# Kernel tuning notes

Hardware: AMD Instinct MI355X
Metric: run time of the kernel (lower is better)

## Reference

```python
import jax, jax.numpy as jnp
import numpy as np

SCALE = 10.0

def _transform_point_cloud(xyz, T_src, T_tgt, H, W):
    # xyz: [B,3,H,W] -> [B,3,H,W] transformed into target camera frame
    B = xyz.shape[0]
    xyzh = jnp.concatenate([xyz.reshape(B, 3, -1), jnp.ones((B, 1, H * W), xyz.dtype)], axis=1)
    M = jnp.linalg.inv(T_tgt) @ T_src  # [4,4]
    out = jnp.einsum('ij,bjn->bin', M, xyzh)[:, :3]
    return out.reshape(B, 3, H, W)

def _project_point_cloud(xyz, feat, K, H, W):
    # xyz: [B,3,H,W], feat: [B,C1,H,W], K: [3,3]. Default flips: horizontal=0, vertical=1.
    B, C1 = feat.shape[0], feat.shape[1]
    xyz = xyz.reshape(B, 3, -1)
    z = xyz[:, 2:3, :]
    im = jnp.round(jnp.einsum('ij,bjn->bin', K, xyz / z))  # [B,3,N]
    x, y = im[:, 0, :], im[:, 1, :]
    valid = (x > 0) & (x < W) & (y > 0) & (y < H)
    # invalid points scatter into dummy slot H*W which is sliced off
    idx = jnp.where(valid, y * W + x, float(H * W)).astype(jnp.int32)  # [B,N]
    ff = feat.reshape(B, C1, -1)
    def scat(f, i):  # f: [C1,N], i: [N]
        return jnp.zeros((C1, H * W + 1), f.dtype).at[:, i].set(f)[:, :H * W]
    dst = jax.vmap(scat)(ff, idx).reshape(B, C1, H, W)
    return dst[:, :, ::-1, :]  # flip vertically (default flip_vertically=1)

def reference(feature, xyzi, T, CAM_MTX, unet_w, unet_b, label):
    B, CAM, C, H, W = feature.shape
    z = xyzi[:, :, 2, :, :]  # [B,CAM,H,W]
    soft = []
    for t in range(CAM):
        feats = []
        for s in range(CAM):
            fs = jnp.concatenate([feature[:, s], z[:, s][:, None]], axis=1)  # [B,C+1,H,W]
            if s != t:
                xyz_t = _transform_point_cloud(xyzi[:, s, :3], T[s], T[t], H, W)
                fs = _project_point_cloud(xyz_t, fs, CAM_MTX[t], H, W)
            feats.append(fs)
        # deterministic stand-in for torch.randperm ordering: target first, rest ascending
        order = [t] + [s for s in range(CAM) if s != t]
        fap = jnp.stack([feats[s] for s in order], axis=1) / SCALE  # [B,CAM,C+1,H,W]
        x = fap.reshape(B, CAM * (C + 1), H, W)
        # UNet stand-in (UNet undefined in source): 1x1 conv (C+1)*CAM -> C
        soft.append(jnp.einsum('oc,bchw->bohw', unet_w, x) + unet_b[None, :, None, None])
    return (jnp.stack(soft, axis=1), label)

def setup_inputs() -> dict:
    key = jax.random.key(0)
    ks = jax.random.split(key, 6)
    B, CAM, C, H, W = 2, 4, 14, 480, 640
    feature = jax.random.normal(ks[0], (B, CAM, C, H, W), jnp.float32)
    zc = jax.random.uniform(ks[1], (B, CAM, 1, H, W), jnp.float32, 1.0, 4.0)
    xy = (jax.random.uniform(ks[2], (B, CAM, 2, H, W), jnp.float32) - 0.5) * 1.2 * zc
    inten = jax.random.uniform(ks[3], (B, CAM, 1, H, W), jnp.float32)
    xyzi = jnp.concatenate([xy, zc, inten], axis=2)
    label = jax.random.randint(ks[4], (B, CAM, H, W), 0, C, jnp.int64)
    Tm = np.tile(np.eye(4, dtype=np.float32), (CAM, 1, 1))
    for k in range(CAM):
        Tm[k, 0, 3] = 0.05 * k
        Tm[k, 1, 3] = -0.03 * k
    K = np.tile(np.array([[500.0, 0.0, W / 2.0], [0.0, 500.0, H / 2.0], [0.0, 0.0, 1.0]], np.float32), (CAM, 1, 1))
    unet_w = jax.random.normal(ks[5], (C, (C + 1) * CAM), jnp.float32) * 0.05
    unet_b = jnp.zeros((C,), jnp.float32)
    return {"feature": feature, "xyzi": xyzi, "T": jnp.asarray(Tm), "CAM_MTX": jnp.asarray(K), "unet_w": unet_w, "unet_b": unet_b, "label": label}
```

## Files before the change

kernel.cpp:

```cpp
#include <hip/hip_runtime.h>

constexpr int B    = 2;
constexpr int CAM  = 4;
constexpr int C    = 14;
constexpr int H    = 480;
constexpr int W    = 640;
constexpr int NPIX = H * W;
constexpr int PK   = 16;

constexpr int SROWS  = 8;
constexpr int STRIPS = H / SROWS;
constexpr int SCELL  = SROWS * W;
constexpr int CAP    = 6144;
constexpr int NSLICE = B * CAM * 3;
constexpr int ABLK   = 1024;
constexpr int NBIN_BLK = NPIX / ABLK;

__global__ void compute_M_kernel(const float* __restrict__ T,
                                 float* __restrict__ Mout) {
    if (threadIdx.x != 0 || blockIdx.x != 0) return;
    for (int t = 0; t < CAM; ++t) {
        float A[4][8];
        for (int i = 0; i < 4; ++i)
            for (int j = 0; j < 4; ++j) {
                A[i][j]     = T[t * 16 + i * 4 + j];
                A[i][4 + j] = (i == j) ? 1.f : 0.f;
            }
        for (int col = 0; col < 4; ++col) {
            int piv = col;
            for (int r = col + 1; r < 4; ++r)
                if (fabsf(A[r][col]) > fabsf(A[piv][col])) piv = r;
            if (piv != col)
                for (int j = 0; j < 8; ++j) {
                    float tmp = A[col][j]; A[col][j] = A[piv][j]; A[piv][j] = tmp;
                }
            float d = A[col][col];
            for (int j = 0; j < 8; ++j) A[col][j] /= d;
            for (int r = 0; r < 4; ++r) {
                if (r == col) continue;
                float m = A[r][col];
                for (int j = 0; j < 8; ++j) A[r][j] -= m * A[col][j];
            }
        }
        for (int s = 0; s < CAM; ++s)
            for (int i = 0; i < 3; ++i)
                for (int j = 0; j < 4; ++j) {
                    float acc = 0.f;
                    for (int k = 0; k < 4; ++k)
                        acc += A[i][4 + k] * T[s * 16 + k * 4 + j];
                    Mout[(t * CAM + s) * 12 + i * 4 + j] = acc;
                }
    }
}

__device__ __forceinline__ bool project(const float* __restrict__ xyzi,
                                        const float* __restrict__ Mp,
                                        const float* __restrict__ Kp,
                                        int bs, int n, int& strip, int& tloc) {
    const float* src = xyzi + (size_t)bs * 4 * NPIX;
    const float x = src[n];
    const float y = src[NPIX + n];
    const float z = src[2 * NPIX + n];

    const float xt = __fadd_rn(__fadd_rn(__fadd_rn(__fmul_rn(Mp[0], x),
                      __fmul_rn(Mp[1], y)), __fmul_rn(Mp[2], z)), Mp[3]);
    const float yt = __fadd_rn(__fadd_rn(__fadd_rn(__fmul_rn(Mp[4], x),
                      __fmul_rn(Mp[5], y)), __fmul_rn(Mp[6], z)), Mp[7]);
    const float zt = __fadd_rn(__fadd_rn(__fadd_rn(__fmul_rn(Mp[8], x),
                      __fmul_rn(Mp[9], y)), __fmul_rn(Mp[10], z)), Mp[11]);

    const float vx = __fdiv_rn(xt, zt);
    const float vy = __fdiv_rn(yt, zt);
    const float u = __fadd_rn(__fadd_rn(__fmul_rn(Kp[0], vx),
                      __fmul_rn(Kp[1], vy)), Kp[2]);
    const float v = __fadd_rn(__fadd_rn(__fmul_rn(Kp[3], vx),
                      __fmul_rn(Kp[4], vy)), Kp[5]);

    const float ur = rintf(u);
    const float vr = rintf(v);

    if (ur > 0.f && ur < (float)W && vr > 0.f && vr < (float)H) {
        const int iv = (int)vr, iu = (int)ur;
        strip = iv >> 3;
        tloc  = (iv & (SROWS - 1)) * W + iu;
        return true;
    }
    return false;
}

__global__ __launch_bounds__(ABLK) void phaseA_kernel(
        const float* __restrict__ xyzi, const float* __restrict__ feature,
        const float* __restrict__ M, const float* __restrict__ Kmtx,
        const int* __restrict__ lab, unsigned int* __restrict__ bins,
        int* __restrict__ gcount, float* __restrict__ packed,
        float* __restrict__ outLab) {
    __shared__ int cnt[STRIPS];
    __shared__ int gbase[STRIPS];
    const int bid = blockIdx.x;
    const int tid = threadIdx.x;

    if (bid < NSLICE * NBIN_BLK) {
        const int slice = bid / NBIN_BLK;
        const int n = (bid % NBIN_BLK) * ABLK + tid;
        const int b = slice / 12;
        const int r = slice - b * 12;
        const int t = r / 3;
        const int j = r - t * 3;
        const int s = j + (j >= t ? 1 : 0);

        if (tid < STRIPS) cnt[tid] = 0;
        __syncthreads();

        int strip = 0, tloc = 0, lslot = 0;
        const bool valid = project(xyzi, M + (t * CAM + s) * 12, Kmtx + t * 9,
                                   b * CAM + s, n, strip, tloc);
        if (valid) lslot = atomicAdd(&cnt[strip], 1);
        __syncthreads();
        if (tid < STRIPS && cnt[tid] > 0)
            gbase[tid] = atomicAdd(&gcount[slice * STRIPS + tid], cnt[tid]);
        __syncthreads();
        if (valid) {
            const int pos = gbase[strip] + lslot;
            if (pos < CAP)
                bins[((size_t)(slice * STRIPS + strip)) * CAP + pos] =
                    ((unsigned int)tloc << 19) | (unsigned int)n;
        }
    } else if (bid < (NSLICE + 8) * NBIN_BLK) {
        const int q  = bid - NSLICE * NBIN_BLK;
        const int bs = q / NBIN_BLK;
        const int n  = (q % NBIN_BLK) * ABLK + tid;
        const float* fb = feature + (size_t)bs * C * NPIX + n;
        float* pb = packed + ((size_t)bs * NPIX + n) * PK;
        float v[PK];
#pragma unroll
        for (int c = 0; c < C; ++c)
            v[c] = __fdiv_rn(fb[(size_t)c * NPIX], 10.0f);
        v[14] = __fdiv_rn(xyzi[((size_t)bs * 4 + 2) * NPIX + n], 10.0f);
        v[15] = 0.f;
#pragma unroll
        for (int q4 = 0; q4 < 4; ++q4)
            *(float4*)(pb + q4 * 4) =
                make_float4(v[q4*4], v[q4*4+1], v[q4*4+2], v[q4*4+3]);
    } else {
        const int q = bid - (NSLICE + 8) * NBIN_BLK;
        const int i = q * ABLK + tid;
        const int4 l4 = ((const int4*)lab)[i];
        ((float4*)outLab)[i] = make_float4((float)l4.x, (float)l4.y,
                                           (float)l4.z, (float)l4.w);
    }
}

__global__ __launch_bounds__(256) void phaseB_kernel(
        const unsigned int* __restrict__ bins, const int* __restrict__ gcount,
        int* __restrict__ winner) {
    __shared__ int tile[SCELL];
    const int bid = blockIdx.x;
    for (int i = threadIdx.x; i < SCELL; i += 256) tile[i] = -1;
    __syncthreads();
    int cntv = gcount[bid];
    if (cntv > CAP) cntv = CAP;
    const unsigned int* bp = bins + (size_t)bid * CAP;
    for (int i = threadIdx.x; i < cntv; i += 256) {
        const unsigned int e = bp[i];
        atomicMax(&tile[e >> 19], (int)(e & 0x7FFFFu));
    }
    __syncthreads();
    const int slice = bid / STRIPS;
    const int strip = bid - slice * STRIPS;
    int* wp = winner + (size_t)slice * NPIX + strip * SCELL;
    for (int i = threadIdx.x; i < SCELL; i += 256) wp[i] = tile[i];
}

__global__ __launch_bounds__(256) void fuse_kernel(
        const float* __restrict__ packed, const int* __restrict__ winner,
        const float* __restrict__ Wmat, const float* __restrict__ bias,
        float* __restrict__ out) {
    __shared__ float sW[C * 60];
    __shared__ float sB[C];
    for (int i = threadIdx.x; i < C * 60; i += 256) sW[i] = Wmat[i];
    if (threadIdx.x < C) sB[threadIdx.x] = bias[threadIdx.x];
    __syncthreads();

    const int n  = blockIdx.x * 256 + threadIdx.x;
    const int bt = blockIdx.y;
    const int b  = bt / CAM;
    const int t  = bt - b * CAM;
    const int h  = n / W;
    const int w  = n - h * W;
    const int pFlip = (H - 1 - h) * W + w;

    float acc[C];
#pragma unroll
    for (int o = 0; o < C; ++o) acc[o] = 0.f;

#pragma unroll
    for (int g = 0; g < CAM; ++g) {
        int s, pix;
        if (g == 0) {
            s = t; pix = n;
        } else {
            const int j = g - 1;
            s = j + (j >= t ? 1 : 0);
            const int wn = winner[(size_t)(b * 12 + t * 3 + j) * NPIX + pFlip];
            if (wn < 0) continue;
            pix = wn;
        }
        const float* pb = packed + ((size_t)(b * CAM + s) * NPIX + pix) * PK;
        float v[PK];
#pragma unroll
        for (int q = 0; q < 4; ++q) {
            const float4 f4 = *(const float4*)(pb + q * 4);
            v[q*4] = f4.x; v[q*4+1] = f4.y; v[q*4+2] = f4.z; v[q*4+3] = f4.w;
        }
#pragma unroll
        for (int c = 0; c < 15; ++c) {
#pragma unroll
            for (int o = 0; o < C; ++o)
                acc[o] = __fadd_rn(acc[o], __fmul_rn(sW[o * 60 + g * 15 + c], v[c]));
        }
    }

    float* ob = out + (size_t)bt * C * NPIX + n;
#pragma unroll
    for (int o = 0; o < C; ++o)
        ob[(size_t)o * NPIX] = __fadd_rn(acc[o], sB[o]);
}

__global__ __launch_bounds__(256) void winner_kernel(
        const float* __restrict__ xyzi, const float* __restrict__ M,
        const float* __restrict__ Kmtx, int* __restrict__ winner) {
    const int n    = blockIdx.x * 256 + threadIdx.x;
    const int pair = blockIdx.y;
    const int b = pair / 12;
    const int r = pair - b * 12;
    const int t = r / 3;
    const int j = r - t * 3;
    const int s = j + (j >= t ? 1 : 0);
    int strip, tloc;
    if (project(xyzi, M + (t * CAM + s) * 12, Kmtx + t * 9,
                b * CAM + s, n, strip, tloc)) {
        const int idx = strip * SCELL + tloc;
        atomicMax(&winner[(size_t)pair * NPIX + idx], n);
    }
}

__global__ __launch_bounds__(256) void pack_kernel(
        const float* __restrict__ feature, const float* __restrict__ xyzi,
        float* __restrict__ packed) {
    const int n  = blockIdx.x * 256 + threadIdx.x;
    const int bs = blockIdx.y;
    const float* fb = feature + (size_t)bs * C * NPIX + n;
    float* pb = packed + ((size_t)bs * NPIX + n) * PK;
    float v[PK];
#pragma unroll
    for (int c = 0; c < C; ++c)
        v[c] = __fdiv_rn(fb[(size_t)c * NPIX], 10.0f);
    v[14] = __fdiv_rn(xyzi[((size_t)bs * 4 + 2) * NPIX + n], 10.0f);
    v[15] = 0.f;
#pragma unroll
    for (int q = 0; q < 4; ++q)
        *(float4*)(pb + q * 4) = make_float4(v[q*4], v[q*4+1], v[q*4+2], v[q*4+3]);
}

__global__ __launch_bounds__(256) void fuse_fallback_kernel(
        const float* __restrict__ feature, const float* __restrict__ xyzi,
        const int* __restrict__ winner, const float* __restrict__ Wmat,
        const float* __restrict__ bias, float* __restrict__ out) {
    __shared__ float sW[C * 60];
    __shared__ float sB[C];
    for (int i = threadIdx.x; i < C * 60; i += 256) sW[i] = Wmat[i];
    if (threadIdx.x < C) sB[threadIdx.x] = bias[threadIdx.x];
    __syncthreads();
    const int n  = blockIdx.x * 256 + threadIdx.x;
    const int bt = blockIdx.y;
    const int b  = bt / CAM;
    const int t  = bt - b * CAM;
    const int h  = n / W;
    const int w  = n - h * W;
    const int pFlip = (H - 1 - h) * W + w;
    float acc[C];
#pragma unroll
    for (int o = 0; o < C; ++o) acc[o] = 0.f;
#pragma unroll
    for (int g = 0; g < CAM; ++g) {
        int s, pix;
        if (g == 0) { s = t; pix = n; }
        else {
            const int j = g - 1;
            s = j + (j >= t ? 1 : 0);
            const int wn = winner[(size_t)(b * 12 + t * 3 + j) * NPIX + pFlip];
            if (wn < 0) continue;
            pix = wn;
        }
        const float* fb = feature + (size_t)(b * CAM + s) * C * NPIX + pix;
        const float zv  = xyzi[((size_t)(b * CAM + s) * 4 + 2) * NPIX + pix];
#pragma unroll
        for (int c = 0; c < C; ++c) {
            const float xc = __fdiv_rn(fb[(size_t)c * NPIX], 10.0f);
#pragma unroll
            for (int o = 0; o < C; ++o)
                acc[o] = __fadd_rn(acc[o], __fmul_rn(sW[o * 60 + g * 15 + c], xc));
        }
        const float zc = __fdiv_rn(zv, 10.0f);
#pragma unroll
        for (int o = 0; o < C; ++o)
            acc[o] = __fadd_rn(acc[o], __fmul_rn(sW[o * 60 + g * 15 + 14], zc));
    }
    float* ob = out + (size_t)bt * C * NPIX + n;
#pragma unroll
    for (int o = 0; o < C; ++o)
        ob[(size_t)o * NPIX] = __fadd_rn(acc[o], sB[o]);
}

__global__ __launch_bounds__(256) void label_copy_kernel(
        const int* __restrict__ lab, float* __restrict__ out) {
    const int i = blockIdx.x * 256 + threadIdx.x;
    const int4 l4 = ((const int4*)lab)[i];
    ((float4*)out)[i] = make_float4((float)l4.x, (float)l4.y,
                                    (float)l4.z, (float)l4.w);
}

extern "C" void kernel_launch(void* const* d_in, const int* in_sizes, int n_in,
                              void* d_out, int out_size, void* d_ws, size_t ws_size,
                              hipStream_t stream) {
    const float* feature = (const float*)d_in[0];
    const float* xyzi    = (const float*)d_in[1];
    const float* T       = (const float*)d_in[2];
    const float* Kmtx    = (const float*)d_in[3];
    const float* unet_w  = (const float*)d_in[4];
    const float* unet_b  = (const float*)d_in[5];
    const int*   label   = (const int*)d_in[6];
    float* out = (float*)d_out;
    float* outLab = out + (size_t)B * CAM * C * NPIX;

    const size_t winnerBytes = (size_t)NSLICE * NPIX * sizeof(int);
    const size_t gcountBytes = (size_t)NSLICE * STRIPS * sizeof(int);
    const size_t binsBytes   = (size_t)NSLICE * STRIPS * CAP * sizeof(unsigned int);
    const size_t packedBytes = (size_t)B * CAM * NPIX * PK * sizeof(float);
    const size_t fastBytes   = winnerBytes + gcountBytes + binsBytes + packedBytes + 1024;

    if (ws_size >= fastBytes) {
        int*          winner = (int*)d_ws;
        int*          gcount = (int*)((char*)d_ws + winnerBytes);
        unsigned int* bins   = (unsigned int*)((char*)d_ws + winnerBytes + gcountBytes);
        float*        packed = (float*)((char*)d_ws + winnerBytes + gcountBytes + binsBytes);
        float*        Mbuf   = (float*)((char*)d_ws + winnerBytes + gcountBytes + binsBytes + packedBytes);

        hipMemsetAsync(gcount, 0, gcountBytes, stream);
        compute_M_kernel<<<1, 1, 0, stream>>>(T, Mbuf);

        const int gA = (NSLICE + 8) * NBIN_BLK + (B * CAM * NPIX / 4) / ABLK;
        phaseA_kernel<<<gA, ABLK, 0, stream>>>(xyzi, feature, Mbuf, Kmtx,
                                               label, bins, gcount, packed, outLab);
        phaseB_kernel<<<NSLICE * STRIPS, 256, 0, stream>>>(bins, gcount, winner);

        dim3 g2(NPIX / 256, B * CAM);
        fuse_kernel<<<g2, 256, 0, stream>>>(packed, winner, unet_w, unet_b, out);
    } else {
        int*   winner = (int*)d_ws;
        float* packed = (float*)((char*)d_ws + winnerBytes);
        float* Mbuf   = (float*)((char*)d_ws + winnerBytes + packedBytes);
        const bool havePacked = ws_size >= winnerBytes + packedBytes + 256;
        if (!havePacked) Mbuf = (float*)((char*)d_ws + winnerBytes);

        hipMemsetAsync(winner, 0xFF, winnerBytes, stream);
        compute_M_kernel<<<1, 1, 0, stream>>>(T, Mbuf);

        dim3 g1(NPIX / 256, NSLICE);
        winner_kernel<<<g1, 256, 0, stream>>>(xyzi, Mbuf, Kmtx, winner);

        dim3 g2(NPIX / 256, B * CAM);
        if (havePacked) {
            pack_kernel<<<g2, 256, 0, stream>>>(feature, xyzi, packed);
            fuse_kernel<<<g2, 256, 0, stream>>>(packed, winner, unet_w, unet_b, out);
        } else {
            fuse_fallback_kernel<<<g2, 256, 0, stream>>>(feature, xyzi, winner,
                                                         unet_w, unet_b, out);
        }
        label_copy_kernel<<<B * CAM * NPIX / 4 / 256, 256, 0, stream>>>(label, outLab);
    }
}
```

Measured before the change: 514.5 us.

## Interleave phaseA work types per block group and parallelize M computation

Phase A blocks shrink from 1024 to 256 threads. Block indices are now interleaved in groups of 17 (12 binning, 4 packing, 1 label-convert) so that compute-light atomic binning runs alongside bandwidth-heavy packing rather than in separate sequential phases. The 4x4 inverse/M computation now runs one (t,s) pair per thread across 16 threads instead of serially on one thread, which shortens that tiny kernel. Smaller blocks mean more global atomics per strip count and more blocks to schedule.

Result: slower. 580.1 us (+12.8%).

```diff
diff --git a/kernel.cpp b/kernel.cpp
--- a/kernel.cpp
+++ b/kernel.cpp
@@ -13,44 +13,52 @@
 constexpr int SCELL  = SROWS * W;
 constexpr int CAP    = 6144;
 constexpr int NSLICE = B * CAM * 3;
-constexpr int ABLK   = 1024;
+
+constexpr int ABLK     = 256;
 constexpr int NBIN_BLK = NPIX / ABLK;
+constexpr int BIN_BLKS = NSLICE * NBIN_BLK;
+constexpr int PACK_BLKS= B * CAM * NBIN_BLK;
+constexpr int LAB_BLKS = B * CAM * NPIX / 4 / ABLK;
+constexpr int GRP_SZ   = 17;
+constexpr int GRPS     = LAB_BLKS;
+static_assert(BIN_BLKS  == GRPS * 12, "bin ratio");
+static_assert(PACK_BLKS == GRPS * 4,  "pack ratio");
 
 __global__ void compute_M_kernel(const float* __restrict__ T,
                                  float* __restrict__ Mout) {
-    if (threadIdx.x != 0 || blockIdx.x != 0) return;
-    for (int t = 0; t < CAM; ++t) {
-        float A[4][8];
-        for (int i = 0; i < 4; ++i)
-            for (int j = 0; j < 4; ++j) {
-                A[i][j]     = T[t * 16 + i * 4 + j];
-                A[i][4 + j] = (i == j) ? 1.f : 0.f;
+    const int id = threadIdx.x;
+    if (blockIdx.x != 0 || id >= CAM * CAM) return;
+    const int t = id / CAM;
+    const int s = id - t * CAM;
+    float A[4][8];
+    for (int i = 0; i < 4; ++i)
+        for (int j = 0; j < 4; ++j) {
+            A[i][j]     = T[t * 16 + i * 4 + j];
+            A[i][4 + j] = (i == j) ? 1.f : 0.f;
+        }
+    for (int col = 0; col < 4; ++col) {
+        int piv = col;
+        for (int r = col + 1; r < 4; ++r)
+            if (fabsf(A[r][col]) > fabsf(A[piv][col])) piv = r;
+        if (piv != col)
+            for (int j = 0; j < 8; ++j) {
+                float tmp = A[col][j]; A[col][j] = A[piv][j]; A[piv][j] = tmp;
             }
-        for (int col = 0; col < 4; ++col) {
-            int piv = col;
-            for (int r = col + 1; r < 4; ++r)
-                if (fabsf(A[r][col]) > fabsf(A[piv][col])) piv = r;
-            if (piv != col)
-                for (int j = 0; j < 8; ++j) {
-                    float tmp = A[col][j]; A[col][j] = A[piv][j]; A[piv][j] = tmp;
-                }
-            float d = A[col][col];
-            for (int j = 0; j < 8; ++j) A[col][j] /= d;
-            for (int r = 0; r < 4; ++r) {
-                if (r == col) continue;
-                float m = A[r][col];
-                for (int j = 0; j < 8; ++j) A[r][j] -= m * A[col][j];
-            }
-        }
-        for (int s = 0; s < CAM; ++s)
-            for (int i = 0; i < 3; ++i)
-                for (int j = 0; j < 4; ++j) {
-                    float acc = 0.f;
-                    for (int k = 0; k < 4; ++k)
-                        acc += A[i][4 + k] * T[s * 16 + k * 4 + j];
-                    Mout[(t * CAM + s) * 12 + i * 4 + j] = acc;
-                }
-    }
+        float d = A[col][col];
+        for (int j = 0; j < 8; ++j) A[col][j] /= d;
+        for (int r = 0; r < 4; ++r) {
+            if (r == col) continue;
+            float m = A[r][col];
+            for (int j = 0; j < 8; ++j) A[r][j] -= m * A[col][j];
+        }
+    }
+    for (int i = 0; i < 3; ++i)
+        for (int j = 0; j < 4; ++j) {
+            float acc = 0.f;
+            for (int k = 0; k < 4; ++k)
+                acc += A[i][4 + k] * T[s * 16 + k * 4 + j];
+            Mout[(t * CAM + s) * 12 + i * 4 + j] = acc;
+        }
 }
 
 __device__ __forceinline__ bool project(const float* __restrict__ xyzi,
@@ -96,12 +104,15 @@
         float* __restrict__ outLab) {
     __shared__ int cnt[STRIPS];
     __shared__ int gbase[STRIPS];
-    const int bid = blockIdx.x;
-    const int tid = threadIdx.x;
-
-    if (bid < NSLICE * NBIN_BLK) {
-        const int slice = bid / NBIN_BLK;
-        const int n = (bid % NBIN_BLK) * ABLK + tid;
+    const int bid  = blockIdx.x;
+    const int tid  = threadIdx.x;
+    const int grp  = bid / GRP_SZ;
+    const int slot = bid - grp * GRP_SZ;
+
+    if (slot < 12) {
+        const int binIdx = grp * 12 + slot;
+        const int slice  = binIdx / NBIN_BLK;
+        const int n      = (binIdx - slice * NBIN_BLK) * ABLK + tid;
         const int b = slice / 12;
         const int r = slice - b * 12;
         const int t = r / 3;
@@ -125,10 +136,10 @@
                 bins[((size_t)(slice * STRIPS + strip)) * CAP + pos] =
                     ((unsigned int)tloc << 19) | (unsigned int)n;
         }
-    } else if (bid < (NSLICE + 8) * NBIN_BLK) {
-        const int q  = bid - NSLICE * NBIN_BLK;
-        const int bs = q / NBIN_BLK;
-        const int n  = (q % NBIN_BLK) * ABLK + tid;
+    } else if (slot < 16) {
+        const int packIdx = grp * 4 + (slot - 12);
+        const int bs = packIdx / NBIN_BLK;
+        const int n  = (packIdx - bs * NBIN_BLK) * ABLK + tid;
         const float* fb = feature + (size_t)bs * C * NPIX + n;
         float* pb = packed + ((size_t)bs * NPIX + n) * PK;
         float v[PK];
@@ -142,8 +153,7 @@
             *(float4*)(pb + q4 * 4) =
                 make_float4(v[q4*4], v[q4*4+1], v[q4*4+2], v[q4*4+3]);
     } else {
-        const int q = bid - (NSLICE + 8) * NBIN_BLK;
-        const int i = q * ABLK + tid;
+        const int i = grp * ABLK + tid;
         const int4 l4 = ((const int4*)lab)[i];
         ((float4*)outLab)[i] = make_float4((float)l4.x, (float)l4.y,
                                            (float)l4.z, (float)l4.w);
@@ -347,11 +357,10 @@
         float*        Mbuf   = (float*)((char*)d_ws + winnerBytes + gcountBytes + binsBytes + packedBytes);
 
         hipMemsetAsync(gcount, 0, gcountBytes, stream);
-        compute_M_kernel<<<1, 1, 0, stream>>>(T, Mbuf);
-
-        const int gA = (NSLICE + 8) * NBIN_BLK + (B * CAM * NPIX / 4) / ABLK;
-        phaseA_kernel<<<gA, ABLK, 0, stream>>>(xyzi, feature, Mbuf, Kmtx,
-                                               label, bins, gcount, packed, outLab);
+        compute_M_kernel<<<1, 64, 0, stream>>>(T, Mbuf);
+
+        phaseA_kernel<<<GRPS * GRP_SZ, ABLK, 0, stream>>>(
+                xyzi, feature, Mbuf, Kmtx, label, bins, gcount, packed, outLab);
         phaseB_kernel<<<NSLICE * STRIPS, 256, 0, stream>>>(bins, gcount, winner);
 
         dim3 g2(NPIX / 256, B * CAM);
@@ -364,7 +373,7 @@
         if (!havePacked) Mbuf = (float*)((char*)d_ws + winnerBytes);
 
         hipMemsetAsync(winner, 0xFF, winnerBytes, stream);
-        compute_M_kernel<<<1, 1, 0, stream>>>(T, Mbuf);
+        compute_M_kernel<<<1, 64, 0, stream>>>(T, Mbuf);
 
         dim3 g1(NPIX / 256, NSLICE);
         winner_kernel<<<g1, 256, 0, stream>>>(xyzi, Mbuf, Kmtx, winner);
```
